# Kernel tuning notes

Hardware: AMD Instinct MI355X
Metric: run time of the kernel (lower is better)

The kernel has to match this reference:

```python
import jax, jax.numpy as jnp
import numpy as np

EPS = 1e-5

def _dh_grid(b):
    # Driscoll-Healy beta grid + quadrature weights (includes sin(beta))
    k = np.arange(2 * b)
    beta = np.pi * (2 * k + 1) / (4 * b)
    j = np.arange(b)
    w = (2.0 / b) * np.sin(beta) * (np.sin(np.outer(beta, 2 * j + 1)) / (2 * j + 1)).sum(1)
    return beta, w

def _wigner_stack(L, betas):
    # d^l_{m m'}(beta) for l<L, zero-padded to slots j=m+(L-1) in a [L,nb,2L-1,2L-1] array.
    betas = np.atleast_1d(np.asarray(betas, np.float64))
    nb = betas.shape[0]
    J = 2 * L - 1
    out = np.zeros((L, nb, J, J), np.float64)
    for l in range(L):
        if l == 0:
            d = np.ones((nb, 1, 1))
        else:
            m = np.arange(-l, l + 1)
            c = np.sqrt(l * (l + 1) - m[:-1] * (m[:-1] + 1.0))
            Jp = np.diag(c, -1).astype(complex)  # raising operator in m=-l..l basis
            Jy = (Jp - Jp.T) / 2j
            ev, V = np.linalg.eigh(Jy)
            ph = np.exp(-1j * betas[:, None] * ev[None, :])
            d = np.einsum('mk,bk,nk->bmn', V, ph, V.conj()).real
        s = (L - 1) - l
        out[l, :, s:s + 2 * l + 1, s:s + 2 * l + 1] = d
    return out

def _constants():
    C = {}
    # layer1: S2 conv b 64 -> 20
    beta1, wq1 = _dh_grid(64)
    d1 = _wigner_stack(20, beta1)
    C['s2_ana'] = jnp.asarray((d1[:, :, :, 19] * wq1[None, :, None] * (2 * np.pi / 128)).astype(np.float32))  # [20,128,39]
    C['half1'] = jnp.asarray(_wigner_stack(20, np.pi / 2)[:, 0, :, 19].astype(np.float32))  # [20,39]
    beta_o1, wq2 = _dh_grid(20)
    ls1 = (2 * np.arange(20) + 1.0)
    C['syn1'] = jnp.asarray((_wigner_stack(20, beta_o1) * ls1[:, None, None, None]).astype(np.float32))  # [20,40,39,39]
    # layer2: SO3 conv b 20 -> 10
    d2 = _wigner_stack(10, beta_o1)
    C['ana2'] = jnp.asarray((d2 * wq2[None, :, None, None] * (2 * np.pi / 40) ** 2).astype(np.float32))  # [10,40,19,19]
    C['half2'] = jnp.asarray(_wigner_stack(10, np.pi / 2)[:, 0].astype(np.float32))  # [10,19,19]
    beta_o2, wq3 = _dh_grid(10)
    ls2 = (2 * np.arange(10) + 1.0)
    C['syn2'] = jnp.asarray((_wigner_stack(10, beta_o2) * ls2[:, None, None, None]).astype(np.float32))  # [10,20,19,19]
    # layer3: SO3 conv b 10 -> 7
    C['ana3'] = jnp.asarray((_wigner_stack(7, beta_o2) * wq3[None, :, None, None] * (2 * np.pi / 20) ** 2).astype(np.float32))  # [7,20,13,13]
    C['half3'] = jnp.asarray(_wigner_stack(7, np.pi / 2)[:, 0].astype(np.float32))  # [7,13,13]
    beta_o3, _ = _dh_grid(7)
    ls3 = (2 * np.arange(7) + 1.0)
    C['syn3'] = jnp.asarray((_wigner_stack(7, beta_o3) * ls3[:, None, None, None]).astype(np.float32))  # [7,14,13,13]
    return C

_C = _constants()

def _so3_ifft(Z, L, d_syn):
    # Z: [L, J, J, B, O] spectral (zero padded); output [B, O, 2L(beta), 2L(alpha), 2L(gamma)]
    M = jnp.einsum('lkjn,ljnbo->bokjn', d_syn, Z)
    N = 2 * L
    J = 2 * L - 1
    idx = (np.arange(J) - (L - 1)) % N
    S = jnp.zeros(M.shape[:3] + (N, N), M.dtype).at[..., idx[:, None], idx[None, :]].set(M)
    return jnp.fft.fft2(S, axes=(-2, -1)).real

def _s2_conv(x, w, bias, C):
    # x: [B, F, 2b_in(beta), 2b_in(alpha)] -> [B, O, 2*20, 2*20, 2*20]
    B, F, K, N = x.shape
    L = 20
    J = 2 * L - 1
    m = np.arange(J) - (L - 1)
    xh = jnp.fft.fft(x, axis=-1)[..., m % N]                       # [B,F,K,J]
    Fx = jnp.einsum('lkj,bfkj->ljbf', C['s2_ana'], xh)             # spherical FFT
    P = w.shape[-1]
    alpha = 2 * np.pi * np.arange(P) / P
    e = jnp.asarray(np.exp(-1j * np.outer(m, alpha)).astype(np.complex64))
    scale = 1.0 / np.sqrt(P * F)
    Ky = jnp.einsum('lj,jp,fop->ljfo', C['half1'], e, w * scale)   # kernel RFT on equatorial grid
    Z = jnp.einsum('ljbf,lnfo->ljnbo', Fx, jnp.conj(Ky))           # s2_mm (outer product over m,n)
    return _so3_ifft(Z, L, C['syn1']) + bias[None, :, None, None, None]

def _so3_conv(x, w, bias, Lo, ana, half, syn):
    # x: [B, F, K(beta), N(alpha), N(gamma)] -> [B, O, 2Lo, 2Lo, 2Lo]
    B, F, K, N, _ = x.shape
    J = 2 * Lo - 1
    m = np.arange(J) - (Lo - 1)
    idx = (-m) % N
    xh = jnp.fft.fft2(x, axes=(-2, -1))[..., idx[:, None], idx[None, :]]  # [B,F,K,J,J]
    Fx = jnp.einsum('lkjn,bfkjn->ljnbf', ana, xh)                  # SO3 FFT
    P = w.shape[-1]
    alpha = 2 * np.pi * np.arange(P) / P
    e = jnp.asarray(np.exp(1j * np.outer(m, alpha)).astype(np.complex64))
    scale = 1.0 / np.sqrt(P * F)
    Ky = jnp.einsum('ljn,jp,fop->ljnfo', half, e, w * scale)       # kernel RFT (beta=pi/2, gamma=0 grid)
    Z = jnp.einsum('ljkbf,lnkfo->ljnbo', Fx, jnp.conj(Ky))         # so3_mm: Z_{mn}=sum_k Fx_{mk} conj(Ky_{nk})
    return _so3_ifft(Z, Lo, syn) + bias[None, :, None, None, None]

def _bn(x, gamma, beta):
    axes = (0,) + tuple(range(2, x.ndim))
    mu = x.mean(axes, keepdims=True)
    var = x.var(axes, keepdims=True)
    shp = (1, -1) + (1,) * (x.ndim - 2)
    return (x - mu) * jax.lax.rsqrt(var + EPS) * gamma.reshape(shp) + beta.reshape(shp)

def _forward(x, w1, b1, g1, bt1, w2, b2, g2, bt2, w3, b3, g3, bt3, w_out, b_out):
    x = _s2_conv(x, w1, b1, _C)
    x = jax.nn.relu(_bn(x, g1, bt1))
    x = _so3_conv(x, w2, b2, 10, _C['ana2'], _C['half2'], _C['syn2'])
    x = jax.nn.relu(_bn(x, g2, bt2))
    x = _so3_conv(x, w3, b3, 7, _C['ana3'], _C['half3'], _C['syn3'])
    x = jax.nn.relu(_bn(x, g3, bt3))
    x = x.reshape(x.shape[0], x.shape[1], -1).max(-1)              # global max pool over SO3 grid
    mu = x.mean(0, keepdims=True)
    var = x.var(0, keepdims=True)
    x = (x - mu) * jax.lax.rsqrt(var + EPS)                        # BatchNorm1d(affine=False)
    x = x @ w_out + b_out
    return jax.nn.log_softmax(x, axis=1)

def setup_inputs():
    key = jax.random.key(0)
    ks = jax.random.split(key, 6)
    B = 16
    return {
        'x': jax.random.normal(ks[0], (B, 6, 128, 128), jnp.float32),
        'w1': jax.random.normal(ks[1], (6, 20, 128), jnp.float32),
        'b1': jnp.zeros((20,), jnp.float32),
        'g1': jnp.ones((20,), jnp.float32),
        'bt1': jnp.zeros((20,), jnp.float32),
        'w2': jax.random.normal(ks[2], (20, 60, 40), jnp.float32),
        'b2': jnp.zeros((60,), jnp.float32),
        'g2': jnp.ones((60,), jnp.float32),
        'bt2': jnp.zeros((60,), jnp.float32),
        'w3': jax.random.normal(ks[3], (60, 100, 20), jnp.float32),
        'b3': jnp.zeros((100,), jnp.float32),
        'g3': jnp.ones((100,), jnp.float32),
        'bt3': jnp.zeros((100,), jnp.float32),
        'w_out': jax.random.normal(ks[4], (100, 55), jnp.float32) * 0.1,
        'b_out': jnp.zeros((55,), jnp.float32),
    }

def reference(x, w1, b1, g1, bt1, w2, b2, g2, bt2, w3, b3, g3, bt3, w_out, b_out):
    return _forward(x, w1, b1, g1, bt1, w2, b2, g2, bt2, w3, b3, g3, bt3, w_out, b_out)
```

## Files before the change

### kernel.cpp

```cpp
#include <hip/hip_runtime.h>
#include <math.h>

#define PI 3.14159265358979323846

__device__ inline int iabs(int x){ return x < 0 ? -x : x; }

__device__ inline void cadd_mul(float2& acc, float2 a, float2 b){
    acc.x += a.x*b.x - a.y*b.y;
    acc.y += a.x*b.y + a.y*b.x;
}
__device__ inline void cadd_mulc(float2& acc, float2 a, float2 b){
    acc.x += a.x*b.x + a.y*b.y;
    acc.y += a.y*b.x - a.x*b.y;
}

__device__ inline double dpowi(double x, int n){
    double r = 1.0;
    for (int i = 0; i < n; ++i) r *= x;
    return r;
}

__device__ double wigner_d(int l, int a, int b, double beta, const double* sf)
{
    double cb = cos(0.5*beta), sb = sin(0.5*beta);
    int smin = max(0, b - a);
    int smax = min(l + b, l - a);
    if (smin > smax) return 0.0;
    double pref = sqrt(sf[l+a]*sf[l-a]*sf[l+b]*sf[l-b]);
    double t = dpowi(cb, 2*l + b - a - 2*smin) * dpowi(sb, a - b + 2*smin);
    if ((a - b + smin) & 1) t = -t;
    double r = -(sb*sb)/(cb*cb);
    double sum = 0.0;
    for (int s = smin; s <= smax; ++s){
        sum += t / (sf[l+b-s]*sf[s]*sf[a-b+s]*sf[l-a-s]);
        t *= r;
    }
    return pref * sum;
}

__global__ void k_wq(double* wq)
{
    int i = blockIdx.x*blockDim.x + threadIdx.x;
    int b, k, off;
    if (i < 128){ b = 64; k = i;      off = 0;   }
    else if (i < 168){ b = 20; k = i-128; off = 128; }
    else if (i < 188){ b = 10; k = i-168; off = 168; }
    else return;
    double beta = PI*(2*k+1)/(4.0*b);
    double s = 0.0;
    for (int j = 0; j < b; ++j) s += sin((2*j+1)*beta)/(2*j+1);
    wq[off+k] = (2.0/b)*sin(beta)*s;
}

__global__ void k_wig_full(float* __restrict__ out, const double* __restrict__ wq,
                           int L, int J, int NB, double denom, double beta_fix,
                           double factor, int mul2l1, int klayout, int jhalf)
{
    __shared__ double sf[40];
    if (threadIdx.x == 0){ sf[0]=1.0; for (int i=1;i<40;i++) sf[i]=sf[i-1]*i; }
    __syncthreads();
    int c0 = (J-1)/2;
    int JROWS = jhalf ? (J+1)/2 : J;
    int idx = blockIdx.x*blockDim.x + threadIdx.x;
    int total = L*NB*JROWS*J;
    if (idx >= total) return;
    int n = idx % J;
    int jj = (idx/J) % JROWS;
    int j = jhalf ? (c0 + jj) : jj;
    int k = (idx/(J*JROWS)) % NB;
    int l = idx/(J*JROWS*NB);
    int mj = j - c0, mn = n - c0;
    float v = 0.f;
    if (iabs(mj) <= l && iabs(mn) <= l){
        double beta = (denom > 0.0) ? PI*(2*k+1)/denom : beta_fix;
        double d = wigner_d(l, mj, mn, beta, sf);
        double mlt = factor * (mul2l1 ? (2.0*l + 1.0) : 1.0);
        if (wq) mlt *= wq[k];
        v = (float)(d*mlt);
    }
    size_t oidx = klayout ? ((size_t)(k*L + l)*J + j)*J + n
                          : ((size_t)(l*NB + k)*J + j)*J + n;
    out[oidx] = v;
}

__global__ void k_wig_col(float* __restrict__ out, const double* __restrict__ wq,
                          int L, int J, int NB, double denom, double beta_fix, double factor,
                          int jhalf)
{
    __shared__ double sf[40];
    if (threadIdx.x == 0){ sf[0]=1.0; for (int i=1;i<40;i++) sf[i]=sf[i-1]*i; }
    __syncthreads();
    int c0 = (J-1)/2;
    int JROWS = jhalf ? (J+1)/2 : J;
    int idx = blockIdx.x*blockDim.x + threadIdx.x;
    int total = L*NB*JROWS;
    if (idx >= total) return;
    int jj = idx % JROWS;
    int j = jhalf ? (c0 + jj) : jj;
    int k = (idx/JROWS) % NB;
    int l = idx/(JROWS*NB);
    int mj = j - c0;
    float v = 0.f;
    if (iabs(mj) <= l){
        double beta = (denom > 0.0) ? PI*(2*k+1)/denom : beta_fix;
        double d = wigner_d(l, mj, 0, beta, sf);
        double mlt = factor;
        if (wq) mlt *= wq[k];
        v = (float)(d*mlt);
    }
    out[(size_t)(l*NB + k)*J + j] = v;
}

__global__ void k_expmat(float2* __restrict__ out, int R, int C, int r0, int c0, int N, double sgn)
{
    int i = blockIdx.x*blockDim.x + threadIdx.x;
    if (i >= R*C) return;
    int c = i % C, r = i / C;
    double ang = sgn*2.0*PI * (double)((r - r0)*(c - c0)) / (double)N;
    out[i] = make_float2((float)cos(ang), (float)sin(ang));
}

__global__ __launch_bounds__(256) void k_dft1(const float* __restrict__ x,
    const float2* __restrict__ E1, float2* __restrict__ xh)
{
    __shared__ float2 sE[4992];
    __shared__ float rows[2048];
    int r0 = blockIdx.x * 16;
    int tid = threadIdx.x;
    for (int i = tid; i < 4992; i += 256) sE[i] = E1[i];
    for (int i = tid; i < 2048; i += 256) rows[i] = x[(size_t)r0*128 + i];
    __syncthreads();
    for (int i = tid; i < 320; i += 256){
        int jj = i % 20, kl = i / 20;
        int j = jj + 19;
        const float* row = &rows[kl*128];
        float2 acc = make_float2(0.f, 0.f);
        for (int a = 0; a < 128; ++a){
            float v = row[a];
            float2 e = sE[a*39 + j];
            acc.x += v*e.x; acc.y += v*e.y;
        }
        xh[(size_t)(r0 + kl)*39 + j] = acc;
    }
}

__global__ void k_fx1(const float* __restrict__ ana, const float2* __restrict__ xh,
                      float2* __restrict__ Fx)
{
    int i = blockIdx.x*blockDim.x + threadIdx.x;
    if (i >= 400) return;
    int hj = i % 20, l = i / 20;
    int j = hj + 19;
    int bf = blockIdx.y;
    const float*  ar = ana + (size_t)l*4992 + j;
    const float2* xr = xh + (size_t)bf*4992 + j;
    float2 acc = make_float2(0.f, 0.f);
    for (int k = 0; k < 128; ++k){
        float a = ar[k*39];
        float2 v = xr[k*39];
        acc.x += a*v.x; acc.y += a*v.y;
    }
    Fx[(size_t)(l*39 + j)*96 + bf] = acc;
}

__global__ void k_wh(float2* __restrict__ wh, const float* __restrict__ w,
                     int J, int P, int F, int O, double sgn)
{
    __shared__ float2 tw[128];
    int tid = threadIdx.x;
    if (tid < P){
        double a = sgn*2.0*PI*tid/P;
        tw[tid] = make_float2((float)cos(a), (float)sin(a));
    }
    __syncthreads();
    int idx = blockIdx.x*blockDim.x + tid;
    if (idx >= J*F*O) return;
    int o = idx % O;
    int f = (idx/O) % F;
    int j = idx/(O*F);
    int mj = j - (J-1)/2;
    int step = ((mj % P) + P) % P;
    const float* wr = w + (f*O+o)*P;
    float2 acc = make_float2(0.f, 0.f);
    int t = 0;
    for (int p = 0; p < P; ++p){
        float v = wr[p];
        acc.x += v*tw[t].x; acc.y += v*tw[t].y;
        t += step; if (t >= P) t -= P;
    }
    wh[idx] = acc;
}

__global__ void k_z1(const float2* __restrict__ Fx, const float2* __restrict__ wh,
                     const float* __restrict__ half1, float2* __restrict__ Z1c, int b0)
{
    int i = blockIdx.x*blockDim.x + threadIdx.x;
    if (i >= 15600) return;
    int bo = blockIdx.y;
    int n = i % 39;
    int lh = i / 39;
    int hj = lh % 20, l = lh / 20;
    int j = hj + 19;
    int b = b0 + bo/20, o = bo % 20;
    float h = half1[l*39 + n] * (1.f/sqrtf(128.f*6.f));
    const float2* fx = Fx + (size_t)(l*39 + j)*96 + b*6;
    const float2* wv = wh + (size_t)n*120 + o;
    float2 acc = make_float2(0.f, 0.f);
    for (int f = 0; f < 6; ++f) cadd_mulc(acc, fx[f], wv[(size_t)f*20]);
    Z1c[(size_t)bo*15600 + i] = make_float2(acc.x*h, acc.y*h);
}

template<int L, int J, int K, int KB, int N, int O, int BS>
__global__ __launch_bounds__(BS) void k_idft_t(const float2* __restrict__ Z,
    const float* __restrict__ syn, const float2* __restrict__ W,
    const float* __restrict__ bias, float* __restrict__ out)
{
    constexpr int JJ = J*J, NN = N*N, c0 = (J-1)/2;
    constexpr int JH = (J+1)/2;
    constexpr int JHJ = JH*J;
    constexpr int LHJ = L*JHJ;
    constexpr int KG = K/KB;
    constexpr int SLOTS = (JHJ + BS - 1)/BS;
    __shared__ float2 sM[KB*JHJ];
    __shared__ float2 sT[JH*N];
    __shared__ float2 sW[J*N];
    int bid = blockIdx.x;
    int kg = bid % KG;
    int bo = bid / KG;
    int k0 = kg*KB;
    int tid = threadIdx.x;

    for (int i = tid; i < J*N; i += BS) sW[i] = W[i];

    float2 acc[SLOTS][KB];
    #pragma unroll
    for (int s = 0; s < SLOTS; ++s)
        #pragma unroll
        for (int kb = 0; kb < KB; ++kb) acc[s][kb] = make_float2(0.f, 0.f);
    #pragma unroll
    for (int s = 0; s < SLOTS; ++s){
        int i = tid + s*BS;
        if (i < JHJ){
            int n = i % J, hj = i / J;
            int lmin = max(hj, iabs(n-c0));
            const float2* zrow = Z + (size_t)bo*LHJ + i;
            const float*  sbase = syn + (size_t)c0*J + i;
            for (int l = lmin; l < L; ++l){
                float2 z = zrow[(size_t)l*JHJ];
                #pragma unroll
                for (int kb = 0; kb < KB; ++kb){
                    float s_ = sbase[(size_t)((k0+kb)*L + l)*JJ];
                    acc[s][kb].x += s_*z.x; acc[s][kb].y += s_*z.y;
                }
            }
        }
    }
    #pragma unroll
    for (int s = 0; s < SLOTS; ++s){
        int i = tid + s*BS;
        if (i < JHJ){
            #pragma unroll
            for (int kb = 0; kb < KB; ++kb) sM[kb*JHJ + i] = acc[s][kb];
        }
    }
    __syncthreads();

    constexpr int RT = (JH+1)/2, CT = N/2;
    for (int kb = 0; kb < KB; ++kb){
        const float2* sMk = &sM[kb*JHJ];
        for (int t = tid; t < RT*CT; t += BS){
            int tg = t % CT, tj = t / CT;
            int h0 = tj*2, g0 = tg*2;
            int h1 = (h0+1 < JH) ? h0+1 : h0;
            float2 a00 = make_float2(0.f,0.f), a01 = make_float2(0.f,0.f);
            float2 a10 = make_float2(0.f,0.f), a11 = make_float2(0.f,0.f);
            for (int n = 0; n < J; ++n){
                float2 w0 = sW[n*N+g0], w1 = sW[n*N+g0+1];
                float2 m0 = sMk[h0*J+n], m1 = sMk[h1*J+n];
                cadd_mul(a00, m0, w0); cadd_mul(a01, m0, w1);
                cadd_mul(a10, m1, w0); cadd_mul(a11, m1, w1);
            }
            sT[h0*N+g0] = a00; sT[h0*N+g0+1] = a01;
            if (h0+1 < JH){ sT[(h0+1)*N+g0] = a10; sT[(h0+1)*N+g0+1] = a11; }
        }
        __syncthreads();
        float bb = bias[bo % O];
        float* obase = out + ((size_t)bo*K + k0 + kb)*NN;
        for (int t = tid; t < CT*CT; t += BS){
            int tg = t % CT, ta = t / CT;
            int a0 = ta*2, g0 = tg*2;
            float2 t00 = sT[g0], t01 = sT[g0+1];
            float r00 = t00.x, r01 = t01.x, r10 = t00.x, r11 = t01.x;
            for (int hj = 1; hj < JH; ++hj){
                float2 wa0 = sW[(c0+hj)*N+a0], wa1 = sW[(c0+hj)*N+a0+1];
                float2 t0 = sT[hj*N+g0], t1 = sT[hj*N+g0+1];
                r00 += 2.f*(t0.x*wa0.x - t0.y*wa0.y);
                r01 += 2.f*(t1.x*wa0.x - t1.y*wa0.y);
                r10 += 2.f*(t0.x*wa1.x - t0.y*wa1.y);
                r11 += 2.f*(t1.x*wa1.x - t1.y*wa1.y);
            }
            obase[(a0+0)*N+g0]   = r00 + bb;
            obase[(a0+0)*N+g0+1] = r01 + bb;
            obase[(a0+1)*N+g0]   = r10 + bb;
            obase[(a0+1)*N+g0+1] = r11 + bb;
        }
        __syncthreads();
    }
}

__global__ __launch_bounds__(256) void k_bn_stats(const float4* __restrict__ x, double* __restrict__ part,
                                                  int B, int C, int S4, int parts)
{
    int c = blockIdx.y, p = blockIdx.x;
    int chunk = (S4 + parts - 1)/parts;
    int s0 = p*chunk, s1e = min(S4, s0 + chunk);
    double a1 = 0.0, a2 = 0.0;
    for (int b = 0; b < B; ++b){
        const float4* base = x + ((size_t)b*C + c)*S4;
        for (int s = s0 + threadIdx.x; s < s1e; s += 256){
            float4 v = base[s];
            a1 += (double)v.x + (double)v.y + (double)v.z + (double)v.w;
            a2 += (double)v.x*v.x + (double)v.y*v.y + (double)v.z*v.z + (double)v.w*v.w;
        }
    }
    __shared__ double r1[256], r2[256];
    r1[threadIdx.x] = a1; r2[threadIdx.x] = a2;
    __syncthreads();
    for (int off = 128; off > 0; off >>= 1){
        if (threadIdx.x < off){ r1[threadIdx.x] += r1[threadIdx.x+off]; r2[threadIdx.x] += r2[threadIdx.x+off]; }
        __syncthreads();
    }
    if (threadIdx.x == 0){ int bid = p*C + c; part[2*bid] = r1[0]; part[2*bid+1] = r2[0]; }
}

__global__ void k_bn_fin(const double* __restrict__ part, const float* __restrict__ g,
                         const float* __restrict__ bt, float2* __restrict__ scsh,
                         int C, int parts, double cnt)
{
    int c = blockIdx.x*blockDim.x + threadIdx.x;
    if (c >= C) return;
    double s1 = 0.0, s2 = 0.0;
    for (int p = 0; p < parts; ++p){ s1 += part[2*(p*C+c)]; s2 += part[2*(p*C+c)+1]; }
    double mu = s1/cnt;
    double var = s2/cnt - mu*mu;
    float sc = (float)(1.0/sqrt(var + 1e-5)) * g[c];
    float sh = bt[c] - (float)mu*sc;
    scsh[c] = make_float2(sc, sh);
}

template<int N, int J>
__global__ __launch_bounds__(256) void k_dft2_t(const float* __restrict__ x, float2* __restrict__ xh,
                                                const float2* __restrict__ EF,
                                                const float2* __restrict__ scsh, int KBETA, int C)
{
    constexpr int JH = (J+1)/2, c0 = (J-1)/2;
    constexpr int NP = N+1;
    __shared__ float tile[N*NP];
    __shared__ float2 sU[JH*N];
    __shared__ float2 sE[N*J];
    int bid = blockIdx.x;
    int tid = threadIdx.x;
    float2 p = scsh[(bid / KBETA) % C];
    const float* src = x + (size_t)bid*N*N;
    for (int i = tid; i < N*N; i += 256){
        int a = i / N, g = i % N;
        tile[a*NP + g] = fmaxf(fmaf(src[i], p.x, p.y), 0.f);
    }
    for (int i = tid; i < N*J; i += 256) sE[i] = EF[i];
    __syncthreads();
    constexpr int HT = (JH+1)/2, GT = N/2;
    for (int t = tid; t < HT*GT; t += 256){
        int tg = t % GT, th = t / GT;
        int h0 = 2*th, g0 = 2*tg;
        int h1 = (h0+1 < JH) ? h0+1 : h0;
        int j0 = c0 + h0, j1 = c0 + h1;
        float2 a00 = make_float2(0.f,0.f), a01 = make_float2(0.f,0.f);
        float2 a10 = make_float2(0.f,0.f), a11 = make_float2(0.f,0.f);
        for (int a = 0; a < N; ++a){
            float v0 = tile[a*NP+g0], v1 = tile[a*NP+g0+1];
            float2 e0 = sE[a*J+j0], e1 = sE[a*J+j1];
            a00.x += v0*e0.x; a00.y += v0*e0.y;
            a01.x += v1*e0.x; a01.y += v1*e0.y;
            a10.x += v0*e1.x; a10.y += v0*e1.y;
            a11.x += v1*e1.x; a11.y += v1*e1.y;
        }
        sU[h0*N+g0] = a00; sU[h0*N+g0+1] = a01;
        if (h0+1 < JH){ sU[(h0+1)*N+g0] = a10; sU[(h0+1)*N+g0+1] = a11; }
    }
    __syncthreads();
    constexpr int NT = (J+1)/2;
    for (int t = tid; t < HT*NT; t += 256){
        int tn = t % NT, th = t / NT;
        int h0 = 2*th, n0 = 2*tn;
        int h1 = (h0+1 < JH) ? h0+1 : h0;
        int n1 = (n0+1 < J) ? n0+1 : n0;
        float2 a00 = make_float2(0.f,0.f), a01 = make_float2(0.f,0.f);
        float2 a10 = make_float2(0.f,0.f), a11 = make_float2(0.f,0.f);
        for (int g = 0; g < N; ++g){
            float2 u0 = sU[h0*N+g], u1 = sU[h1*N+g];
            float2 e0 = sE[g*J+n0], e1 = sE[g*J+n1];
            cadd_mul(a00, u0, e0); cadd_mul(a01, u0, e1);
            cadd_mul(a10, u1, e0); cadd_mul(a11, u1, e1);
        }
        float2* d0 = xh + (size_t)bid*J*J + (size_t)(c0+h0)*J;
        d0[n0] = a00;
        if (n0+1 < J) d0[n0+1] = a01;
        if (h0+1 < JH){
            float2* d1 = xh + (size_t)bid*J*J + (size_t)(c0+h0+1)*J;
            d1[n0] = a10;
            if (n0+1 < J) d1[n0+1] = a11;
        }
    }
}

__global__ void k_fx(const float* __restrict__ ana, const float2* __restrict__ xh,
                     float2* __restrict__ Fx, int L, int J, int JH, int K, int BF)
{
    int i = blockIdx.x*blockDim.x + threadIdx.x;
    int JJ = J*J;
    int total = L*JH*J;
    if (i >= total) return;
    int bf = blockIdx.y;
    int n = i % J;
    int hj = (i / J) % JH;
    int l = i / (J*JH);
    int c0 = (J-1)/2;
    int jn = (c0+hj)*J + n;
    const float*  ar = ana + (size_t)l*K*JJ + jn;
    const float2* xr = xh + (size_t)bf*K*JJ + jn;
    float2 acc = make_float2(0.f, 0.f);
    for (int k = 0; k < K; ++k){
        float a = ar[(size_t)k*JJ];
        float2 v = xr[(size_t)k*JJ];
        acc.x += a*v.x; acc.y += a*v.y;
    }
    Fx[((size_t)l*JJ + jn)*BF + bf] = acc;
}

__global__ void k_h(const float* __restrict__ half, const float2* __restrict__ Fx,
                    float2* __restrict__ H, int L, int J, int JH, int BF)
{
    int idx = blockIdx.x*blockDim.x + threadIdx.x;
    int total = L*JH*J*BF;
    if (idx >= total) return;
    int bf = idx % BF;
    int n = (idx/BF) % J;
    int hj = (idx/(BF*J)) % JH;
    int l = idx/(BF*J*JH);
    int c0 = (J-1)/2;
    int j = c0 + hj;
    const float* hr = half + (l*J+n)*J;
    const float2* fr = Fx + (size_t)(l*J+j)*J*BF + bf;
    float2 acc = make_float2(0.f, 0.f);
    for (int k = 0; k < J; ++k){
        float h = hr[k];
        float2 v = fr[(size_t)k*BF];
        acc.x += h*v.x; acc.y += h*v.y;
    }
    H[((size_t)(l*J+j)*J + n)*BF + bf] = acc;
}

__global__ __launch_bounds__(256) void k_zg(const float2* __restrict__ H,
    const float2* __restrict__ wh, float2* __restrict__ Z,
    int L, int J, int JH, int B, int F, int O, float scale)
{
    extern __shared__ float2 smem[];
    float2* swh = smem;
    float2* sH  = smem + F*O;
    int n = blockIdx.x;
    int b = blockIdx.y;
    int tid = threadIdx.x;
    int c0 = (J-1)/2;
    int LH = L*JH;
    int FO = F*O;
    const float2* whn = wh + (size_t)n*FO;
    for (int i = tid; i < FO; i += 256) swh[i] = whn[i];
    for (int i = tid; i < LH*F; i += 256){
        int f = i % F, lh = i / F;
        int l = lh / JH, hj = lh % JH;
        int lj = l*J + c0 + hj;
        sH[f*LH + lh] = H[((size_t)(lj*J + n)*B + b)*F + f];
    }
    __syncthreads();
    int total = O*LH;
    for (int i = tid; i < total; i += 256){
        int lh = i % LH, o = i / LH;
        float2 acc = make_float2(0.f, 0.f);
        for (int f = 0; f < F; ++f)
            cadd_mulc(acc, sH[f*LH + lh], swh[f*O + o]);
        Z[(size_t)(b*O + o)*LH*J + (size_t)lh*J + n] = make_float2(acc.x*scale, acc.y*scale);
    }
}

__global__ void k_pool(const float* __restrict__ x, float* __restrict__ pooled, int S,
                       const float2* __restrict__ scsh, int C)
{
    int bid = blockIdx.x;
    float2 p = scsh[bid % C];
    const float* base = x + (long long)bid*S;
    float m = 0.f;
    for (int i = threadIdx.x; i < S; i += blockDim.x)
        m = fmaxf(m, fmaf(base[i], p.x, p.y));
    __shared__ float r[256];
    r[threadIdx.x] = m;
    __syncthreads();
    for (int off = 128; off > 0; off >>= 1){
        if (threadIdx.x < off) r[threadIdx.x] = fmaxf(r[threadIdx.x], r[threadIdx.x+off]);
        __syncthreads();
    }
    if (threadIdx.x == 0) pooled[bid] = fmaxf(r[0], 0.f);
}

__global__ __launch_bounds__(256) void k_final(const float* __restrict__ pooled,
    const float* __restrict__ w, const float* __restrict__ bias, float* __restrict__ out)
{
    __shared__ float pn[1600];
    __shared__ float z[880];
    int tid = threadIdx.x;
    for (int f = tid; f < 100; f += 256){
        float s1 = 0.f, s2 = 0.f;
        for (int b = 0; b < 16; ++b){ float v = pooled[b*100+f]; s1 += v; s2 += v*v; }
        float mu = s1/16.f;
        float var = s2/16.f - mu*mu;
        float inv = rsqrtf(var + 1e-5f);
        for (int b = 0; b < 16; ++b) pn[b*100+f] = (pooled[b*100+f]-mu)*inv;
    }
    __syncthreads();
    for (int i = tid; i < 880; i += 256){
        int c = i % 55, b = i/55;
        float acc = bias[c];
        for (int f = 0; f < 100; ++f) acc += pn[b*100+f]*w[f*55+c];
        z[i] = acc;
    }
    __syncthreads();
    for (int b = tid; b < 16; b += 256){
        float m = -1e30f;
        for (int c = 0; c < 55; ++c) m = fmaxf(m, z[b*55+c]);
        float s = 0.f;
        for (int c = 0; c < 55; ++c) s += expf(z[b*55+c]-m);
        float lse = m + logf(s);
        for (int c = 0; c < 55; ++c) out[b*55+c] = z[b*55+c]-lse;
    }
}

static inline int cdiv(long long a, long long b){ return (int)((a + b - 1)/b); }

extern "C" void kernel_launch(void* const* d_in, const int* in_sizes, int n_in,
                              void* d_out, int out_size, void* d_ws, size_t ws_size,
                              hipStream_t stream)
{
    (void)in_sizes; (void)n_in; (void)out_size; (void)ws_size;
    const float* x   = (const float*)d_in[0];
    const float* w1  = (const float*)d_in[1];
    const float* b1  = (const float*)d_in[2];
    const float* g1  = (const float*)d_in[3];
    const float* bt1 = (const float*)d_in[4];
    const float* w2  = (const float*)d_in[5];
    const float* b2  = (const float*)d_in[6];
    const float* g2  = (const float*)d_in[7];
    const float* bt2 = (const float*)d_in[8];
    const float* w3  = (const float*)d_in[9];
    const float* b3  = (const float*)d_in[10];
    const float* g3  = (const float*)d_in[11];
    const float* bt3 = (const float*)d_in[12];
    const float* wo  = (const float*)d_in[13];
    const float* bo  = (const float*)d_in[14];
    float* out = (float*)d_out;
    float* ws  = (float*)d_ws;

    const size_t O_WQ    = 0;
    const size_t O_S2ANA = 376;
    const size_t O_HALF1 = 100216;
    const size_t O_SYN1  = 100996;
    const size_t O_ANA2  = 1317796;
    const size_t O_HALF2 = 1462196;
    const size_t O_SYN2  = 1465806;
    const size_t O_ANA3  = 1538006;
    const size_t O_HALF3 = 1561666;
    const size_t O_SYN3  = 1562849;
    const size_t O_STATS = 1579412;
    const size_t O_PART  = 1580132;
    const size_t O_EF2   = O_PART + 8192;
    const size_t O_EF3   = O_PART + 9712;
    const size_t O_POOL  = 1596516;
    const size_t O_XH1   = 1598116;
    const size_t O_FX1   = 2556580;
    const size_t O_WH1   = 2706340;
    const size_t O_WH2   = 2715700;
    const size_t O_WH3   = 2761300;
    const size_t O_W1    = 2917300;
    const size_t O_W2    = 2920420;
    const size_t O_W3    = 2921180;
    const size_t O_E1    = 2921544;
    const size_t O_A1    = 2931528;
    const size_t O_A2    = 23411528;

    double* WQd   = (double*)(ws + O_WQ);
    float*  S2ANA = ws + O_S2ANA;
    float*  HALF1 = ws + O_HALF1;
    float*  SYN1  = ws + O_SYN1;
    float*  ANA2  = ws + O_ANA2;
    float*  HALF2 = ws + O_HALF2;
    float*  SYN2  = ws + O_SYN2;
    float*  ANA3  = ws + O_ANA3;
    float*  HALF3 = ws + O_HALF3;
    float*  SYN3  = ws + O_SYN3;
    float2* SCSH  = (float2*)(ws + O_STATS);
    double* PART  = (double*)(ws + O_PART);
    float2* EF2   = (float2*)(ws + O_EF2);
    float2* EF3   = (float2*)(ws + O_EF3);
    float*  POOLED= ws + O_POOL;
    float2* XH1   = (float2*)(ws + O_XH1);
    float2* FX1   = (float2*)(ws + O_FX1);
    float2* WH1   = (float2*)(ws + O_WH1);
    float2* WH2   = (float2*)(ws + O_WH2);
    float2* WH3   = (float2*)(ws + O_WH3);
    float2* W1    = (float2*)(ws + O_W1);
    float2* W2    = (float2*)(ws + O_W2);
    float2* W3    = (float2*)(ws + O_W3);
    float2* E1    = (float2*)(ws + O_E1);
    float*  X1    = ws + O_A1;
    float2* FX2   = (float2*)(ws + O_A1);
    float2* H2    = (float2*)(ws + O_A1 + 2310400);
    float2* Z2    = (float2*)(ws + O_A1 + 4620800);
    float2* XH3   = (float2*)(ws + O_A1);
    float2* FX3   = (float2*)(ws + O_A1 + 6489600);
    float2* H3    = (float2*)(ws + O_A1 + 8760960);
    float2* Z3    = (float2*)(ws + O_A1 + 11032320);
    float2* Z1C   = (float2*)(ws + O_A2);
    float2* XH2   = (float2*)(ws + O_A2);
    float*  X2    = ws + O_A2;
    float*  X3    = ws + O_A2;

    const double F128 = 2.0*PI/128.0;
    const double F40sq = (2.0*PI/40.0)*(2.0*PI/40.0);
    const double F20sq = (2.0*PI/20.0)*(2.0*PI/20.0);

    k_wq<<<1, 256, 0, stream>>>(WQd);
    k_wig_col <<<cdiv(20*128*20,256),256,0,stream>>>(S2ANA, WQd,     20, 39, 128, 256.0, 0.0,   F128, 1);
    k_wig_col <<<cdiv(20*39,256),    256,0,stream>>>(HALF1, nullptr, 20, 39, 1,   0.0,   PI/2,  1.0,  0);
    k_wig_full<<<cdiv(624000,256),   256,0,stream>>>(SYN1,  nullptr, 20, 39, 40,  80.0,  0.0,   1.0,   1, 1, 1);
    k_wig_full<<<cdiv(76000,256),    256,0,stream>>>(ANA2,  WQd+128, 10, 19, 40,  80.0,  0.0,   F40sq, 0, 0, 1);
    k_wig_full<<<cdiv(3610,256),     256,0,stream>>>(HALF2, nullptr, 10, 19, 1,   0.0,   PI/2,  1.0,   0, 0, 0);
    k_wig_full<<<cdiv(38000,256),    256,0,stream>>>(SYN2,  nullptr, 10, 19, 20,  40.0,  0.0,   1.0,   1, 1, 1);
    k_wig_full<<<cdiv(12740,256),    256,0,stream>>>(ANA3,  WQd+168, 7,  13, 20,  40.0,  0.0,   F20sq, 0, 0, 1);
    k_wig_full<<<cdiv(1183,256),     256,0,stream>>>(HALF3, nullptr, 7,  13, 1,   0.0,   PI/2,  1.0,   0, 0, 0);
    k_wig_full<<<cdiv(8918,256),     256,0,stream>>>(SYN3,  nullptr, 7,  13, 14,  28.0,  0.0,   1.0,   1, 1, 1);
    k_expmat  <<<cdiv(1560,256),256,0,stream>>>(W1, 39, 40, 19, 0, 40, -1.0);
    k_expmat  <<<cdiv(380,256), 256,0,stream>>>(W2, 19, 20,  9, 0, 20, -1.0);
    k_expmat  <<<cdiv(182,256), 256,0,stream>>>(W3, 13, 14,  6, 0, 14, -1.0);
    k_expmat  <<<cdiv(4992,256),256,0,stream>>>(E1, 128, 39, 0, 19, 128, -1.0);
    k_expmat  <<<cdiv(760,256), 256,0,stream>>>(EF2, 40, 19, 0, 9, 40, +1.0);
    k_expmat  <<<cdiv(260,256), 256,0,stream>>>(EF3, 20, 13, 0, 6, 20, +1.0);

    k_dft1<<<768,256,0,stream>>>(x, E1, XH1);
    k_fx1 <<<dim3(2,96),256,0,stream>>>(S2ANA, XH1, FX1);
    k_wh  <<<cdiv(4680,256),  256,0,stream>>>(WH1, w1, 39, 128, 6, 20, -1.0);
    k_wh  <<<cdiv(22800,256), 256,0,stream>>>(WH2, w2, 19, 40, 20, 60, +1.0);
    k_wh  <<<cdiv(78000,256), 256,0,stream>>>(WH3, w3, 13, 20, 60, 100, +1.0);
    for (int c = 0; c < 2; ++c){
        int b0 = c*8;
        k_z1<<<dim3(cdiv(15600,256),160),256,0,stream>>>(FX1, WH1, HALF1, Z1C, b0);
        k_idft_t<20,39,40,2,40,20,256><<<160*20,256,0,stream>>>(Z1C, SYN1, W1, b1, X1 + (size_t)b0*20*64000);
    }
    k_bn_stats<<<dim3(32,20),256,0,stream>>>((const float4*)X1, PART, 16, 20, 16000, 32);
    k_bn_fin  <<<1,256,0,stream>>>(PART, g1, bt1, SCSH, 20, 32, 16.0*64000.0);

    k_dft2_t<40,19><<<12800,256,0,stream>>>(X1, XH2, EF2, SCSH, 40, 20);
    k_fx  <<<dim3(cdiv(1900,256),320),256,0,stream>>>(ANA2, XH2, FX2, 10, 19, 10, 40, 320);
    k_h   <<<cdiv(608000,256),256,0,stream>>>(HALF2, FX2, H2, 10, 19, 10, 320);
    k_zg  <<<dim3(19,16),256,(1200+2000)*sizeof(float2),stream>>>(H2, WH2, Z2, 10, 19, 10, 16, 20, 60, 1.f/sqrtf(800.f));
    k_idft_t<10,19,20,5,20,60,256><<<960*4,256,0,stream>>>(Z2, SYN2, W2, b2, X2);
    k_bn_stats<<<dim3(8,60),256,0,stream>>>((const float4*)X2, PART, 16, 60, 2000, 8);
    k_bn_fin  <<<1,256,0,stream>>>(PART, g2, bt2, SCSH+20, 60, 8, 16.0*8000.0);

    k_dft2_t<20,13><<<19200,256,0,stream>>>(X2, XH3, EF3, SCSH+20, 20, 60);
    k_fx  <<<dim3(cdiv(637,256),960),256,0,stream>>>(ANA3, XH3, FX3, 7, 13, 7, 20, 960);
    k_h   <<<cdiv(611520,256),256,0,stream>>>(HALF3, FX3, H3, 7, 13, 7, 960);
    k_zg  <<<dim3(13,16),256,(6000+2940)*sizeof(float2),stream>>>(H3, WH3, Z3, 7, 13, 7, 16, 60, 100, 1.f/sqrtf(1200.f));
    k_idft_t<7,13,14,7,14,100,256><<<1600*2,256,0,stream>>>(Z3, SYN3, W3, b3, X3);
    k_bn_stats<<<dim3(8,100),256,0,stream>>>((const float4*)X3, PART, 16, 100, 686, 8);
    k_bn_fin  <<<1,256,0,stream>>>(PART, g3, bt3, SCSH+80, 100, 8, 16.0*2744.0);

    k_pool <<<1600,256,0,stream>>>(X3, POOLED, 2744, SCSH+80, 100);
    k_final<<<1,256,0,stream>>>(POOLED, wo, bo, out);
}
```

Baseline: 937.8 us.

## Pack layer-1 Z coefficients triangularly and process full batch in one launch

k_z1 now skips the (l,hj,n) entries that are structurally zero and stores only the valid ones in a packed triangular layout of 5530 entries per batch-output pair instead of 15600. k_idft_t gains a PACKED template path that walks this layout with incremental address arithmetic. The two-chunk batch loop is replaced by single launches over all 16 batches, which needs Z1C big enough for all 320 pairs. The aim is less Z traffic and footprint, fewer launches and larger grids. The cost is less regular, uncoalesced z loads in the packed walk.

```diff
diff --git a/kernel.cpp b/kernel.cpp
--- a/kernel.cpp
+++ b/kernel.cpp
@@ -4,6 +4,10 @@
 #define PI 3.14159265358979323846
 
 __device__ inline int iabs(int x){ return x < 0 ? -x : x; }
+
+__device__ __host__ constexpr int packed_off(int l){
+    return ((l-1)*l*(2*l-1))/3 + (3*l*(l-1))/2 + l;
+}
 
 __device__ inline void cadd_mul(float2& acc, float2 a, float2 b){
     acc.x += a.x*b.x - a.y*b.y;
@@ -192,7 +196,7 @@
 }
 
 __global__ void k_z1(const float2* __restrict__ Fx, const float2* __restrict__ wh,
-                     const float* __restrict__ half1, float2* __restrict__ Z1c, int b0)
+                     const float* __restrict__ half1, float2* __restrict__ Z1c)
 {
     int i = blockIdx.x*blockDim.x + threadIdx.x;
     if (i >= 15600) return;
@@ -200,17 +204,19 @@
     int n = i % 39;
     int lh = i / 39;
     int hj = lh % 20, l = lh / 20;
+    if (hj > l || iabs(n - 19) > l) return;
     int j = hj + 19;
-    int b = b0 + bo/20, o = bo % 20;
+    int b = bo/20, o = bo % 20;
     float h = half1[l*39 + n] * (1.f/sqrtf(128.f*6.f));
     const float2* fx = Fx + (size_t)(l*39 + j)*96 + b*6;
     const float2* wv = wh + (size_t)n*120 + o;
     float2 acc = make_float2(0.f, 0.f);
     for (int f = 0; f < 6; ++f) cadd_mulc(acc, fx[f], wv[(size_t)f*20]);
-    Z1c[(size_t)bo*15600 + i] = make_float2(acc.x*h, acc.y*h);
-}
-
-template<int L, int J, int K, int KB, int N, int O, int BS>
+    int pidx = packed_off(l) + hj*(2*l+1) + (n - 19 + l);
+    Z1c[(size_t)bo*5530 + pidx] = make_float2(acc.x*h, acc.y*h);
+}
+
+template<int L, int J, int K, int KB, int N, int O, int BS, int PACKED>
 __global__ __launch_bounds__(BS) void k_idft_t(const float2* __restrict__ Z,
     const float* __restrict__ syn, const float2* __restrict__ W,
     const float* __restrict__ bias, float* __restrict__ out)
@@ -219,6 +225,7 @@
     constexpr int JH = (J+1)/2;
     constexpr int JHJ = JH*J;
     constexpr int LHJ = L*JHJ;
+    constexpr int PTOT = packed_off(L);
     constexpr int KG = K/KB;
     constexpr int SLOTS = (JHJ + BS - 1)/BS;
     __shared__ float2 sM[KB*JHJ];
@@ -243,14 +250,28 @@
         if (i < JHJ){
             int n = i % J, hj = i / J;
             int lmin = max(hj, iabs(n-c0));
-            const float2* zrow = Z + (size_t)bo*LHJ + i;
             const float*  sbase = syn + (size_t)c0*J + i;
-            for (int l = lmin; l < L; ++l){
-                float2 z = zrow[(size_t)l*JHJ];
-                #pragma unroll
-                for (int kb = 0; kb < KB; ++kb){
-                    float s_ = sbase[(size_t)((k0+kb)*L + l)*JJ];
-                    acc[s][kb].x += s_*z.x; acc[s][kb].y += s_*z.y;
+            if (PACKED){
+                const float2* zb = Z + (size_t)bo*PTOT;
+                int addr = packed_off(lmin) + hj*(2*lmin+1) + (n - c0 + lmin);
+                for (int l = lmin; l < L; ++l){
+                    float2 z = zb[addr];
+                    addr += (l+1)*(2*l+1) + 2*hj + 1;
+                    #pragma unroll
+                    for (int kb = 0; kb < KB; ++kb){
+                        float s_ = sbase[(size_t)((k0+kb)*L + l)*JJ];
+                        acc[s][kb].x += s_*z.x; acc[s][kb].y += s_*z.y;
+                    }
+                }
+            } else {
+                const float2* zrow = Z + (size_t)bo*LHJ + i;
+                for (int l = lmin; l < L; ++l){
+                    float2 z = zrow[(size_t)l*JHJ];
+                    #pragma unroll
+                    for (int kb = 0; kb < KB; ++kb){
+                        float s_ = sbase[(size_t)((k0+kb)*L + l)*JJ];
+                        acc[s][kb].x += s_*z.x; acc[s][kb].y += s_*z.y;
+                    }
                 }
             }
         }
@@ -658,11 +679,8 @@
     k_wh  <<<cdiv(4680,256),  256,0,stream>>>(WH1, w1, 39, 128, 6, 20, -1.0);
     k_wh  <<<cdiv(22800,256), 256,0,stream>>>(WH2, w2, 19, 40, 20, 60, +1.0);
     k_wh  <<<cdiv(78000,256), 256,0,stream>>>(WH3, w3, 13, 20, 60, 100, +1.0);
-    for (int c = 0; c < 2; ++c){
-        int b0 = c*8;
-        k_z1<<<dim3(cdiv(15600,256),160),256,0,stream>>>(FX1, WH1, HALF1, Z1C, b0);
-        k_idft_t<20,39,40,2,40,20,256><<<160*20,256,0,stream>>>(Z1C, SYN1, W1, b1, X1 + (size_t)b0*20*64000);
-    }
+    k_z1  <<<dim3(cdiv(15600,256),320),256,0,stream>>>(FX1, WH1, HALF1, Z1C);
+    k_idft_t<20,39,40,2,40,20,256,1><<<320*20,256,0,stream>>>(Z1C, SYN1, W1, b1, X1);
     k_bn_stats<<<dim3(32,20),256,0,stream>>>((const float4*)X1, PART, 16, 20, 16000, 32);
     k_bn_fin  <<<1,256,0,stream>>>(PART, g1, bt1, SCSH, 20, 32, 16.0*64000.0);
 
@@ -670,7 +688,7 @@
     k_fx  <<<dim3(cdiv(1900,256),320),256,0,stream>>>(ANA2, XH2, FX2, 10, 19, 10, 40, 320);
     k_h   <<<cdiv(608000,256),256,0,stream>>>(HALF2, FX2, H2, 10, 19, 10, 320);
     k_zg  <<<dim3(19,16),256,(1200+2000)*sizeof(float2),stream>>>(H2, WH2, Z2, 10, 19, 10, 16, 20, 60, 1.f/sqrtf(800.f));
-    k_idft_t<10,19,20,5,20,60,256><<<960*4,256,0,stream>>>(Z2, SYN2, W2, b2, X2);
+    k_idft_t<10,19,20,5,20,60,256,0><<<960*4,256,0,stream>>>(Z2, SYN2, W2, b2, X2);
     k_bn_stats<<<dim3(8,60),256,0,stream>>>((const float4*)X2, PART, 16, 60, 2000, 8);
     k_bn_fin  <<<1,256,0,stream>>>(PART, g2, bt2, SCSH+20, 60, 8, 16.0*8000.0);
 
@@ -678,7 +696,7 @@
     k_fx  <<<dim3(cdiv(637,256),960),256,0,stream>>>(ANA3, XH3, FX3, 7, 13, 7, 20, 960);
     k_h   <<<cdiv(611520,256),256,0,stream>>>(HALF3, FX3, H3, 7, 13, 7, 960);
     k_zg  <<<dim3(13,16),256,(6000+2940)*sizeof(float2),stream>>>(H3, WH3, Z3, 7, 13, 7, 16, 60, 100, 1.f/sqrtf(1200.f));
-    k_idft_t<7,13,14,7,14,100,256><<<1600*2,256,0,stream>>>(Z3, SYN3, W3, b3, X3);
+    k_idft_t<7,13,14,7,14,100,256,0><<<1600*2,256,0,stream>>>(Z3, SYN3, W3, b3, X3);
     k_bn_stats<<<dim3(8,100),256,0,stream>>>((const float4*)X3, PART, 16, 100, 686, 8);
     k_bn_fin  <<<1,256,0,stream>>>(PART, g3, bt3, SCSH+80, 100, 8, 16.0*2744.0);
 
```

Measured after the change: 874.8 us. 1.07x faster.
